# Kernel optimization log

Measured on AMD Instinct MI355X. Metric: run time of the kernel, lower is better.

Reference implementation:

```python
import jax, jax.numpy as jnp
import numpy as np

T = 0.07          # cfg.CAP.TEMP
K = 50            # cfg.CAP.HARD_NEG_K
LOSS_WEIGHT = 0.5 # cfg.CAP.LOSS_WEIGHT
C_CAM = 8         # number of cameras
P = 2048          # pseudo-ID classes per camera bank


def setup_inputs() -> dict:
    key = jax.random.key(0)
    k1, k2, k3, k4 = jax.random.split(key, 4)
    B, D = 256, 2048
    inputs = jax.random.normal(k1, (B, D), jnp.float32)
    labels = jax.random.randint(k2, (B,), 0, P)
    cams = jax.random.randint(k3, (B,), 0, C_CAM)
    tempV = jax.random.normal(k4, (C_CAM * P, D), jnp.float32)
    tempV = tempV / jnp.linalg.norm(tempV, axis=1, keepdims=True)  # memory rows are L2-normalized
    return {"inputs": inputs, "labels": labels, "cams": cams, "tempV": tempV}


def _seg_mean_sum(vals, cams):
    # original loops over unique cams: loss += mean(vals within cam); empty cams contribute 0
    sums = jax.ops.segment_sum(vals, cams, num_segments=C_CAM)
    cnts = jax.ops.segment_sum(jnp.ones_like(vals), cams, num_segments=C_CAM)
    return jnp.sum(jnp.where(cnts > 0, sums / jnp.maximum(cnts, 1.0), 0.0))


def reference(inputs, labels, cams, tempV):
    B = inputs.shape[0]
    # cfg.CAP.NORM_FEAT
    x = inputs / jnp.linalg.norm(inputs, axis=1, keepdims=True)

    # one fused matmul against the concatenated memory; per-camera banks are contiguous P-slices
    all_logits = x @ tempV.T                      # [B, C_CAM*P]
    logits3 = all_logits.reshape(B, C_CAM, P)

    # ---- intra-camera loss: logits against the sample's own camera bank ----
    percam = jnp.take_along_axis(logits3, cams[:, None, None], axis=1)[:, 0, :] / T  # [B, P]
    lse_i = jax.scipy.special.logsumexp(percam, axis=1)
    ce = lse_i - jnp.take_along_axis(percam, labels[:, None], axis=1)[:, 0]
    loss_intra = _seg_mean_sum(ce, cams)

    # ---- inter-camera loss with hard-negative mining ----
    rows = jnp.arange(B)[:, None]
    # each ID has one centroid in every camera bank: positions label + P*cam
    ori_ind = labels[:, None] + P * jnp.arange(C_CAM)[None, :]        # [B, C_CAM]
    sims = all_logits.at[rows, ori_ind].set(-10000.0)                 # mask positives
    _, sel_ind = jax.lax.top_k(sims, K)                               # hard negatives (== sort[-K:])
    ori_logits = jnp.take_along_axis(all_logits, ori_ind, axis=1) / T  # [B, C_CAM]
    sel_logits = jnp.take_along_axis(all_logits, sel_ind, axis=1) / T  # [B, K]
    cat = jnp.concatenate([ori_logits, sel_logits], axis=1)            # [B, C_CAM+K]
    lse_c = jax.scipy.special.logsumexp(cat, axis=1)
    # target = 1/len(ori) on positives, 0 on negatives -> lse - mean(positive logits)
    loss_k = lse_c - jnp.mean(ori_logits, axis=1)
    loss_inter = LOSS_WEIGHT * _seg_mean_sum(loss_k, cams)

    return (loss_intra, loss_inter)
```

## Files before the change

### kernel.cpp

```cpp
#include <hip/hip_runtime.h>
#include <hip/hip_bf16.h>

#define BATCH 256
#define DIM   2048
#define NMEM  16384
#define PCLS  2048
#define CCAM  8
#define KSEL  50
#define T_INV 14.285714285714285714f
#define NB2   2048

typedef __bf16 bf16x8 __attribute__((ext_vector_type(8)));
typedef float  f32x4  __attribute__((ext_vector_type(4)));

static __device__ __forceinline__ unsigned int f2bf(float f) {
  unsigned int u = __float_as_uint(f);
  return (u + 0x7FFFu + ((u >> 16) & 1u)) >> 16;
}
static __device__ __forceinline__ unsigned int pk2(float lo, float hi) {
  return f2bf(lo) | (f2bf(hi) << 16);
}
static __device__ __forceinline__ int binw(float x, float lo, float scale) {
  int b = (int)((x - lo) * scale);
  return b > (NB2 - 1) ? (NB2 - 1) : b;
}

static __device__ __forceinline__ size_t pa_idx(int r, int c) {
  return (size_t)(r >> 4) * (size_t)(64 * 8 * (DIM / 32))
       + (size_t)(c >> 5) * 512
       + (size_t)(((r & 15) | (((c >> 3) & 3) << 4))) * 8
       + (size_t)(c & 7);
}

__global__ __launch_bounds__(256) void norm_cast_kernel(
    const float* __restrict__ in, unsigned short* __restrict__ xpk) {
  __shared__ float red[256];
  const int b = blockIdx.x, t = threadIdx.x;
  const float4* row = (const float4*)(in + (size_t)b * DIM);
  float4 a0 = row[t];
  float4 a1 = row[t + 256];
  float ss = a0.x*a0.x + a0.y*a0.y + a0.z*a0.z + a0.w*a0.w
           + a1.x*a1.x + a1.y*a1.y + a1.z*a1.z + a1.w*a1.w;
  red[t] = ss; __syncthreads();
  for (int s = 128; s > 0; s >>= 1) { if (t < s) red[t] += red[t + s]; __syncthreads(); }
  const float rn = rsqrtf(red[0]);
  ushort4 o0, o1;
  o0.x = (unsigned short)f2bf(a0.x*rn); o0.y = (unsigned short)f2bf(a0.y*rn);
  o0.z = (unsigned short)f2bf(a0.z*rn); o0.w = (unsigned short)f2bf(a0.w*rn);
  o1.x = (unsigned short)f2bf(a1.x*rn); o1.y = (unsigned short)f2bf(a1.y*rn);
  o1.z = (unsigned short)f2bf(a1.z*rn); o1.w = (unsigned short)f2bf(a1.w*rn);
  *(ushort4*)&xpk[pa_idx(b, 4 * t)]         = o0;
  *(ushort4*)&xpk[pa_idx(b, 4 * (t + 256))] = o1;
}

#define BMH 128
#define BNW 64
#define BKC 64
#define NCH (DIM / BKC)

__global__ __launch_bounds__(256, 2) void gemm_kernel(
    const unsigned short* __restrict__ Xpk,
    const float* __restrict__ V,
    float* __restrict__ C) {
  __shared__ __align__(16) unsigned short Bf[2][8][512];
  const int t    = threadIdx.x;
  const int lane = t & 63;
  const int wid  = t >> 6;
  const int widM = wid >> 1, widN = wid & 1;
  const int n0 = blockIdx.x * BNW;
  const int m0 = blockIdx.y * BMH;

  const int vr  = t >> 2;
  const int vc4 = (t & 3) * 4;
  const float* Vp = V + (size_t)(n0 + vr) * DIM + vc4;
  const int wfr = vr & 15, wjn = vr >> 4;

  const unsigned short* Apk = Xpk + (size_t)((m0 >> 4) + widM * 4) * 32768
                                  + (size_t)lane * 8;

  f32x4 acc[4][2];
#pragma unroll
  for (int i = 0; i < 4; i++)
#pragma unroll
    for (int j = 0; j < 2; j++) acc[i][j] = (f32x4){0.f, 0.f, 0.f, 0.f};

  bf16x8 aA[8], aB[8];
  float4 vA[4], vB[4];

#define LOADV(VS, ch)                                                         \
  {                                                                           \
    const int ck_ = (ch);                                                     \
    _Pragma("unroll")                                                         \
    for (int g = 0; g < 4; ++g)                                               \
      VS[g] = *(const float4*)(Vp + ck_ * BKC + g * 16);                      \
  }
#define LOADA(AS, ch)                                                         \
  {                                                                           \
    const int ck_ = (ch);                                                     \
    _Pragma("unroll")                                                         \
    for (int i = 0; i < 4; ++i)                                               \
      _Pragma("unroll")                                                       \
      for (int s = 0; s < 2; ++s)                                             \
        AS[i * 2 + s] = *(const bf16x8*)(Apk + (size_t)i * 32768              \
                                             + (size_t)(ck_ * 2 + s) * 512);  \
  }
#define WRITEB(buf, VS)                                                       \
  {                                                                           \
    _Pragma("unroll")                                                         \
    for (int g = 0; g < 4; ++g) {                                             \
      const int c_  = vc4 + g * 16;                                           \
      const int f_  = wjn * 2 + (c_ >> 5);                                    \
      const int sl_ = (((c_ & 31) >> 3) << 4) + wfr;                          \
      uint2 p_; p_.x = pk2(VS[g].x, VS[g].y); p_.y = pk2(VS[g].z, VS[g].w);   \
      *(uint2*)&Bf[buf][f_][sl_ * 8 + (c_ & 7)] = p_;                         \
    }                                                                         \
  }
#define COMPUTE(buf, AS)                                                      \
  {                                                                           \
    bf16x8 bF_[2][2];                                                         \
    _Pragma("unroll")                                                         \
    for (int j = 0; j < 2; ++j)                                               \
      _Pragma("unroll")                                                       \
      for (int s = 0; s < 2; ++s)                                             \
        bF_[j][s] = *(const bf16x8*)&Bf[buf][(widN * 2 + j) * 2 + s]          \
                                       [(size_t)lane * 8];                    \
    asm volatile("s_waitcnt vmcnt(12) lgkmcnt(0)" ::: "memory");              \
    __builtin_amdgcn_sched_barrier(0);                                        \
    _Pragma("unroll")                                                         \
    for (int s = 0; s < 2; ++s)                                               \
      _Pragma("unroll")                                                       \
      for (int i = 0; i < 4; ++i)                                             \
        _Pragma("unroll")                                                     \
        for (int j = 0; j < 2; ++j)                                           \
          acc[i][j] = __builtin_amdgcn_mfma_f32_16x16x32_bf16(                \
              AS[i * 2 + s], bF_[j][s], acc[i][j], 0, 0, 0);                  \
  }

  {
    float4 v0[4];
    LOADV(v0, 0);
    asm volatile("s_waitcnt vmcnt(0)" ::: "memory");
    WRITEB(0, v0);
  }
  LOADV(vA, 1);
  LOADA(aA, 0);
  asm volatile("s_waitcnt lgkmcnt(0)" ::: "memory");
  __builtin_amdgcn_s_barrier();

#pragma unroll 1
  for (int it = 0; it < NCH / 2; ++it) {
    const int P0 = 2 * it;
    LOADV(vB, min(P0 + 2, NCH - 1));
    LOADA(aB, min(P0 + 1, NCH - 1));
    COMPUTE(0, aA);
    WRITEB(1, vA);
    asm volatile("s_waitcnt lgkmcnt(0)" ::: "memory");
    __builtin_amdgcn_s_barrier();
    LOADV(vA, min(P0 + 3, NCH - 1));
    LOADA(aA, min(P0 + 2, NCH - 1));
    COMPUTE(1, aB);
    WRITEB(0, vB);
    asm volatile("s_waitcnt lgkmcnt(0)" ::: "memory");
    __builtin_amdgcn_s_barrier();
  }

  const int cr = (lane >> 4) * 4;
  const int cc = lane & 15;
#pragma unroll
  for (int i = 0; i < 4; i++)
#pragma unroll
    for (int j = 0; j < 2; j++)
#pragma unroll
      for (int r = 0; r < 4; r++)
        C[(size_t)(m0 + widM * 64 + i * 16 + cr + r) * NMEM
          + (n0 + widN * 32 + j * 16 + cc)] = acc[i][j][r];
#undef LOADV
#undef LOADA
#undef WRITEB
#undef COMPUTE
}

__global__ __launch_bounds__(1024) void row_loss_kernel(
    const float* __restrict__ logits,
    const int* __restrict__ labels, const int* __restrict__ cams,
    float* __restrict__ ce_out, float* __restrict__ lossk_out) {
  __shared__ float ovs[CCAM];
  __shared__ float wredA[16], wredB[16];
  __shared__ int   hist[NB2];
  __shared__ int   pint[256];
  __shared__ float bl[512];
  __shared__ int   bcount;
  __shared__ int   bstar_s, cabove_s, totwin_s;
  __shared__ float vmax_s;

  const int b = blockIdx.x, t = threadIdx.x;
  const int lane = t & 63, wid = t >> 6;
  const int cam = cams[b], label = labels[b];
  const float* row = logits + (size_t)b * NMEM;

  if (t < CCAM) ovs[t] = row[t * PCLS + label];

  float4 rr[4];
#pragma unroll
  for (int i = 0; i < 4; i++) rr[i] = *(const float4*)(row + (size_t)(t + 1024 * i) * 4);

  float vmax = -1e30f, Si = 0.f;
#pragma unroll
  for (int i = 0; i < 4; i++) {
    const int base = (t + 1024 * i) * 4;
    const float xs[4] = {rr[i].x, rr[i].y, rr[i].z, rr[i].w};
#pragma unroll
    for (int e = 0; e < 4; e++) {
      const int n = base + e;
      const float x = xs[e];
      if ((n >> 11) == cam) Si += __expf(x * T_INV);
      if ((n & (PCLS - 1)) != label) vmax = fmaxf(vmax, x);
    }
  }
#pragma unroll
  for (int off = 32; off > 0; off >>= 1) {
    vmax = fmaxf(vmax, __shfl_down(vmax, off));
    Si  += __shfl_down(Si, off);
  }
  if (lane == 0) { wredA[wid] = vmax; wredB[wid] = Si; }
  __syncthreads();
  if (t == 0) {
    float m = -1e30f, s = 0.f;
    for (int i = 0; i < 16; i++) { m = fmaxf(m, wredA[i]); s += wredB[i]; }
    vmax_s = m;
    ce_out[b] = logf(s) - ovs[cam] * T_INV;
    bcount = 0;
  }
  __syncthreads();

  float W = 0.0625f;
  float lo = 0.f, scale = 0.f;
  for (int att = 0; att < 6; ++att) {
    __syncthreads();
    for (int i = t; i < NB2; i += 1024) hist[i] = 0;
    __syncthreads();
    lo = vmax_s - W; scale = (float)NB2 / W;
#pragma unroll
    for (int i = 0; i < 4; i++) {
      const int base = (t + 1024 * i) * 4;
      const float xs[4] = {rr[i].x, rr[i].y, rr[i].z, rr[i].w};
#pragma unroll
      for (int e = 0; e < 4; e++) {
        const int n = base + e;
        const float x = xs[e];
        if (((n & (PCLS - 1)) != label) && x >= lo)
          atomicAdd(&hist[binw(x, lo, scale)], 1);
      }
    }
    __syncthreads();
    if (t < 256) {
      int ps = 0;
#pragma unroll
      for (int i = 0; i < 8; i++) ps += hist[t * 8 + i];
      pint[t] = ps;
    }
    __syncthreads();
    if (t == 0) {
      int tot = 0;
      for (int i = 0; i < 256; i++) tot += pint[i];
      totwin_s = tot;
      if (tot >= KSEL) {
        int cum = 0, bstar = 0, cab = 0;
        for (int tc = 255; tc >= 0; tc--) {
          if (cum + pint[tc] >= KSEL) {
            for (int bi = tc * 8 + 7; bi >= tc * 8; bi--) {
              int h = hist[bi];
              if (cum + h >= KSEL) { bstar = bi; cab = cum; break; }
              cum += h;
            }
            break;
          }
          cum += pint[tc];
        }
        bstar_s = bstar; cabove_s = cab;
      }
    }
    __syncthreads();
    if (totwin_s >= KSEL) break;
    W *= 8.f;
  }
  const int bstar = bstar_s;

  float S2 = 0.f;
#pragma unroll
  for (int i = 0; i < 4; i++) {
    const int base = (t + 1024 * i) * 4;
    const float xs[4] = {rr[i].x, rr[i].y, rr[i].z, rr[i].w};
#pragma unroll
    for (int e = 0; e < 4; e++) {
      const int n = base + e;
      const float x = xs[e];
      if (((n & (PCLS - 1)) != label) && x >= lo) {
        const int bin = binw(x, lo, scale);
        if (bin > bstar) S2 += __expf(x * T_INV);
        else if (bin == bstar) {
          int p = atomicAdd(&bcount, 1);
          if (p < 512) bl[p] = x;
        }
      }
    }
  }
#pragma unroll
  for (int off = 32; off > 0; off >>= 1) S2 += __shfl_down(S2, off);
  if (lane == 0) wredB[wid] = S2;
  __syncthreads();

  if (t == 0) {
    float S2tot = 0.f;
    for (int i = 0; i < 16; i++) S2tot += wredB[i];
    const int need = KSEL - cabove_s;
    const int bc = min(bcount, 512);
    for (int r = 0; r < need; r++) {
      float mx = -1e30f; int mi = 0;
      for (int i = 0; i < bc; i++) if (bl[i] > mx) { mx = bl[i]; mi = i; }
      S2tot += __expf(mx * T_INV);
      bl[mi] = -1e30f;
    }
    float sumo = 0.f;
#pragma unroll
    for (int c = 0; c < CCAM; c++) { S2tot += __expf(ovs[c] * T_INV); sumo += ovs[c]; }
    lossk_out[b] = logf(S2tot) - (sumo * T_INV) * (1.0f / CCAM);
  }
}

__global__ __launch_bounds__(256) void finalize_kernel(
    const float* __restrict__ ce, const float* __restrict__ lossk,
    const int* __restrict__ cams, float* __restrict__ out) {
  __shared__ float ce_s[BATCH], lk_s[BATCH];
  __shared__ int   cam_s[BATCH];
  __shared__ float si[CCAM], sk[CCAM], cnt[CCAM];
  const int t = threadIdx.x;
  ce_s[t]  = ce[t];
  lk_s[t]  = lossk[t];
  cam_s[t] = cams[t];
  __syncthreads();
  if (t < CCAM) {
    float a = 0.f, b = 0.f; int n = 0;
    for (int i = 0; i < BATCH; i++) {
      if (cam_s[i] == t) { a += ce_s[i]; b += lk_s[i]; n++; }
    }
    si[t] = a; sk[t] = b; cnt[t] = (float)n;
  }
  __syncthreads();
  if (t == 0) {
    float li = 0.f, lk = 0.f;
    for (int c = 0; c < CCAM; c++) {
      if (cnt[c] > 0.f) { li += si[c] / cnt[c]; lk += sk[c] / cnt[c]; }
    }
    out[0] = li;
    out[1] = 0.5f * lk;
  }
}

extern "C" void kernel_launch(void* const* d_in, const int* in_sizes, int n_in,
                              void* d_out, int out_size, void* d_ws, size_t ws_size,
                              hipStream_t stream) {
  const float* inputs = (const float*)d_in[0];
  const int*   labels = (const int*)d_in[1];
  const int*   cams   = (const int*)d_in[2];
  const float* tempV  = (const float*)d_in[3];
  float* out = (float*)d_out;

  char* ws = (char*)d_ws;
  unsigned short* xpk = (unsigned short*)ws;
  float* logits       = (float*)(ws + (1u << 20));
  float* ce           = (float*)(ws + (1u << 20) + (16u << 20));
  float* lossk        = (float*)(ws + (1u << 20) + (16u << 20) + 1024);

  norm_cast_kernel<<<BATCH, 256, 0, stream>>>(inputs, xpk);
  gemm_kernel<<<dim3(NMEM / BNW, BATCH / BMH), 256, 0, stream>>>(xpk, tempV, logits);
  row_loss_kernel<<<BATCH, 1024, 0, stream>>>(logits, labels, cams, ce, lossk);
  finalize_kernel<<<1, 256, 0, stream>>>(ce, lossk, cams, out);
}
```

Before: 257.3 us.

## Cover full batch per GEMM block to read each memory row once

Reshapes the GEMM tile from 128x64 over a 2D grid to 256x32 over a 1D grid, so each block computes all batch rows for a narrower slice of memory columns. Each fp32 tempV row is now loaded and bf16-converted by a single block instead of two, removing duplicate global reads of the large memory bank. The LDS B layout, per-thread load mapping and wait counts are adjusted to match. Each block does less conversion work per MFMA, but the A operand is reloaded across more blocks.

```diff
diff --git a/kernel.cpp b/kernel.cpp
--- a/kernel.cpp
+++ b/kernel.cpp
@@ -53,8 +53,7 @@
   *(ushort4*)&xpk[pa_idx(b, 4 * (t + 256))] = o1;
 }
 
-#define BMH 128
-#define BNW 64
+#define BNW 32
 #define BKC 64
 #define NCH (DIM / BKC)
 
@@ -62,20 +61,20 @@
     const unsigned short* __restrict__ Xpk,
     const float* __restrict__ V,
     float* __restrict__ C) {
-  __shared__ __align__(16) unsigned short Bf[2][8][512];
+  __shared__ __align__(16) unsigned short Bf[2][2][2][64][8];
   const int t    = threadIdx.x;
   const int lane = t & 63;
   const int wid  = t >> 6;
-  const int widM = wid >> 1, widN = wid & 1;
   const int n0 = blockIdx.x * BNW;
-  const int m0 = blockIdx.y * BMH;
-
-  const int vr  = t >> 2;
-  const int vc4 = (t & 3) * 4;
-  const float* Vp = V + (size_t)(n0 + vr) * DIM + vc4;
-  const int wfr = vr & 15, wjn = vr >> 4;
-
-  const unsigned short* Apk = Xpk + (size_t)((m0 >> 4) + widM * 4) * 32768
+
+  const int vn = t >> 3;
+  const int vc = (t & 7) * 4;
+  const float* Vp = V + (size_t)(n0 + vn) * DIM + vc;
+  const int w_nf   = vn >> 4;
+  const int w_slot = (vn & 15) | (((t & 7) >> 1) << 4);
+  const int w_elem = ((t & 7) & 1) * 4;
+
+  const unsigned short* Apk = Xpk + (size_t)(wid * 4) * 32768
                                   + (size_t)lane * 8;
 
   f32x4 acc[4][2];
@@ -85,14 +84,13 @@
     for (int j = 0; j < 2; j++) acc[i][j] = (f32x4){0.f, 0.f, 0.f, 0.f};
 
   bf16x8 aA[8], aB[8];
-  float4 vA[4], vB[4];
-
-#define LOADV(VS, ch)                                                         \
+  float4 vA0, vA1, vB0, vB1;
+
+#define LOADV(V0, V1, ch)                                                     \
   {                                                                           \
     const int ck_ = (ch);                                                     \
-    _Pragma("unroll")                                                         \
-    for (int g = 0; g < 4; ++g)                                               \
-      VS[g] = *(const float4*)(Vp + ck_ * BKC + g * 16);                      \
+    V0 = *(const float4*)(Vp + ck_ * BKC);                                    \
+    V1 = *(const float4*)(Vp + ck_ * BKC + 32);                               \
   }
 #define LOADA(AS, ch)                                                         \
   {                                                                           \
@@ -104,16 +102,13 @@
         AS[i * 2 + s] = *(const bf16x8*)(Apk + (size_t)i * 32768              \
                                              + (size_t)(ck_ * 2 + s) * 512);  \
   }
-#define WRITEB(buf, VS)                                                       \
+#define WRITEB(buf, V0, V1)                                                   \
   {                                                                           \
-    _Pragma("unroll")                                                         \
-    for (int g = 0; g < 4; ++g) {                                             \
-      const int c_  = vc4 + g * 16;                                           \
-      const int f_  = wjn * 2 + (c_ >> 5);                                    \
-      const int sl_ = (((c_ & 31) >> 3) << 4) + wfr;                          \
-      uint2 p_; p_.x = pk2(VS[g].x, VS[g].y); p_.y = pk2(VS[g].z, VS[g].w);   \
-      *(uint2*)&Bf[buf][f_][sl_ * 8 + (c_ & 7)] = p_;                         \
-    }                                                                         \
+    uint2 p0_, p1_;                                                           \
+    p0_.x = pk2(V0.x, V0.y); p0_.y = pk2(V0.z, V0.w);                         \
+    p1_.x = pk2(V1.x, V1.y); p1_.y = pk2(V1.z, V1.w);                         \
+    *(uint2*)&Bf[buf][w_nf][0][w_slot][w_elem] = p0_;                         \
+    *(uint2*)&Bf[buf][w_nf][1][w_slot][w_elem] = p1_;                         \
   }
 #define COMPUTE(buf, AS)                                                      \
   {                                                                           \
@@ -122,9 +117,8 @@
     for (int j = 0; j < 2; ++j)                                               \
       _Pragma("unroll")                                                       \
       for (int s = 0; s < 2; ++s)                                             \
-        bF_[j][s] = *(const bf16x8*)&Bf[buf][(widN * 2 + j) * 2 + s]          \
-                                       [(size_t)lane * 8];                    \
-    asm volatile("s_waitcnt vmcnt(12) lgkmcnt(0)" ::: "memory");              \
+        bF_[j][s] = *(const bf16x8*)&Bf[buf][j][s][lane][0];                  \
+    asm volatile("s_waitcnt vmcnt(10) lgkmcnt(0)" ::: "memory");              \
     __builtin_amdgcn_sched_barrier(0);                                        \
     _Pragma("unroll")                                                         \
     for (int s = 0; s < 2; ++s)                                               \
@@ -136,13 +130,10 @@
               AS[i * 2 + s], bF_[j][s], acc[i][j], 0, 0, 0);                  \
   }
 
-  {
-    float4 v0[4];
-    LOADV(v0, 0);
-    asm volatile("s_waitcnt vmcnt(0)" ::: "memory");
-    WRITEB(0, v0);
-  }
-  LOADV(vA, 1);
+  LOADV(vA0, vA1, 0);
+  asm volatile("s_waitcnt vmcnt(0)" ::: "memory");
+  WRITEB(0, vA0, vA1);
+  LOADV(vA0, vA1, 1);
   LOADA(aA, 0);
   asm volatile("s_waitcnt lgkmcnt(0)" ::: "memory");
   __builtin_amdgcn_s_barrier();
@@ -150,16 +141,16 @@
 #pragma unroll 1
   for (int it = 0; it < NCH / 2; ++it) {
     const int P0 = 2 * it;
-    LOADV(vB, min(P0 + 2, NCH - 1));
+    LOADV(vB0, vB1, min(P0 + 2, NCH - 1));
     LOADA(aB, min(P0 + 1, NCH - 1));
     COMPUTE(0, aA);
-    WRITEB(1, vA);
+    WRITEB(1, vA0, vA1);
     asm volatile("s_waitcnt lgkmcnt(0)" ::: "memory");
     __builtin_amdgcn_s_barrier();
-    LOADV(vA, min(P0 + 3, NCH - 1));
+    LOADV(vA0, vA1, min(P0 + 3, NCH - 1));
     LOADA(aA, min(P0 + 2, NCH - 1));
     COMPUTE(1, aB);
-    WRITEB(0, vB);
+    WRITEB(0, vB0, vB1);
     asm volatile("s_waitcnt lgkmcnt(0)" ::: "memory");
     __builtin_amdgcn_s_barrier();
   }
@@ -172,8 +163,8 @@
     for (int j = 0; j < 2; j++)
 #pragma unroll
       for (int r = 0; r < 4; r++)
-        C[(size_t)(m0 + widM * 64 + i * 16 + cr + r) * NMEM
-          + (n0 + widN * 32 + j * 16 + cc)] = acc[i][j][r];
+        C[(size_t)(wid * 64 + i * 16 + cr + r) * NMEM
+          + (n0 + j * 16 + cc)] = acc[i][j][r];
 #undef LOADV
 #undef LOADA
 #undef WRITEB
@@ -373,7 +364,7 @@
   float* lossk        = (float*)(ws + (1u << 20) + (16u << 20) + 1024);
 
   norm_cast_kernel<<<BATCH, 256, 0, stream>>>(inputs, xpk);
-  gemm_kernel<<<dim3(NMEM / BNW, BATCH / BMH), 256, 0, stream>>>(xpk, tempV, logits);
+  gemm_kernel<<<NMEM / BNW, 256, 0, stream>>>(xpk, tempV, logits);
   row_loss_kernel<<<BATCH, 1024, 0, stream>>>(logits, labels, cams, ce, lossk);
   finalize_kernel<<<1, 256, 0, stream>>>(ce, lossk, cams, out);
 }
```

New measurement: 260.5 us. No clear change (+1.2%).
